# Kernel tuning notes

Hardware: AMD Instinct MI355X
Metric: run time of the kernel (lower is better)

Reference implementation:

```python
import jax, jax.numpy as jnp
import numpy as np

N_NODES = 100000
N_EDGES = 1600000
NUM_GRAPHS = 128


def _gcn_layer(x, W, b, senders, receivers, n_node):
    # Linear transform first (cheaper: feature dim small)
    x = x @ W + b  # [N, out]
    ones = jnp.ones(senders.shape[0], dtype=x.dtype)
    deg_s = jax.ops.segment_sum(ones, senders, n_node)     # out-degree
    deg_r = jax.ops.segment_sum(ones, receivers, n_node)   # in-degree
    # symmetric normalization: D^-1/2 A D^-1/2
    x = x * jax.lax.rsqrt(jnp.maximum(deg_s, 1.0))[:, None]
    x = jax.ops.segment_sum(x[senders], receivers, n_node)  # gather-scatter aggregation
    x = x * jax.lax.rsqrt(jnp.maximum(deg_r, 1.0))[:, None]
    return x


def setup_inputs() -> dict:
    key = jax.random.key(0)
    ks = jax.random.split(key, 10)
    x = jax.random.normal(ks[0], (N_NODES, 9), dtype=jnp.float32)
    senders = jax.random.randint(ks[1], (N_EDGES,), 0, N_NODES)
    receivers = jax.random.randint(ks[2], (N_EDGES,), 0, N_NODES)
    batch = jnp.sort(jax.random.randint(ks[3], (N_NODES,), 0, NUM_GRAPHS))
    # learned params (Dense: W [in,out], b [out]) with LeCun-normal-ish scale
    def dense(k, din, dout):
        return jax.random.normal(k, (din, dout), dtype=jnp.float32) / np.sqrt(din)
    W1 = dense(ks[4], 9, 64)
    b1 = jnp.zeros((64,), jnp.float32)
    W2 = dense(ks[5], 64, 128)
    b2 = jnp.zeros((128,), jnp.float32)
    W3 = dense(ks[6], 128, 2)
    b3 = jnp.zeros((2,), jnp.float32)
    return {"x": x, "senders": senders, "receivers": receivers, "batch": batch,
            "num_graphs": NUM_GRAPHS, "W1": W1, "b1": b1, "W2": W2, "b2": b2,
            "W3": W3, "b3": b3}


def reference(x, senders, receivers, batch, num_graphs, W1, b1, W2, b2, W3, b3):
    n_node = x.shape[0]
    x = jax.nn.relu(_gcn_layer(x, W1, b1, senders, receivers, n_node))
    x = jax.nn.relu(_gcn_layer(x, W2, b2, senders, receivers, n_node))
    x = _gcn_layer(x, W3, b3, senders, receivers, n_node)
    # graph-level pooling
    return jax.ops.segment_sum(x, batch, num_graphs)
```

## Files before the change

### kernel.cpp

```cpp
#include <hip/hip_runtime.h>
#include <hip/hip_bf16.h>
#include <cstddef>

#define NBMAX 512
#define BCAP 5120
#define BKCHUNK 3200

typedef unsigned short bf16t;
typedef __attribute__((ext_vector_type(8))) short short8;
typedef __attribute__((ext_vector_type(4))) float f32x4;

static __device__ __forceinline__ float2 up2(unsigned u) {
    return make_float2(__uint_as_float(u << 16), __uint_as_float(u & 0xffff0000u));
}
static __device__ __forceinline__ bf16t f2bf(float f) {
    unsigned u = __float_as_uint(f);
    u += 0x7fffu + ((u >> 16) & 1u);
    return (bf16t)(u >> 16);
}
static __device__ __forceinline__ unsigned pk2(float a, float b) {
    return (unsigned)f2bf(a) | ((unsigned)f2bf(b) << 16);
}

__global__ void k_bucket(const int* __restrict__ S, const int* __restrict__ R,
                         unsigned* __restrict__ bufR, unsigned char* __restrict__ bufS,
                         int* __restrict__ gCntR, int* __restrict__ gCntS,
                         const float* __restrict__ W2, bf16t* __restrict__ W2f,
                         int nE, int nB) {
    __shared__ int histR[NBMAX], lstR[NBMAX], baseR[NBMAX];
    __shared__ int histS[NBMAX], lstS[NBMAX], baseS[NBMAX];
    __shared__ int sm[256];
    __shared__ unsigned sortedR[BKCHUNK];
    __shared__ unsigned short bOfR[BKCHUNK];
    __shared__ unsigned char sortedS[BKCHUNK];
    __shared__ unsigned short bOfS[BKCHUNK];
    int t = threadIdx.x;
    int nSort = gridDim.x - 4;
    if (blockIdx.x >= nSort) {
        int tt = (blockIdx.x - nSort) * blockDim.x + t;
        if (tt < 1024) {
            int nt = tt >> 7, kh = (tt >> 6) & 1, lane = tt & 63;
            int n = nt * 16 + (lane & 15);
            int k0 = kh * 32 + (lane >> 4) * 8;
            uint4 p;
            p.x = pk2(W2[(k0 + 0) * 128 + n], W2[(k0 + 1) * 128 + n]);
            p.y = pk2(W2[(k0 + 2) * 128 + n], W2[(k0 + 3) * 128 + n]);
            p.z = pk2(W2[(k0 + 4) * 128 + n], W2[(k0 + 5) * 128 + n]);
            p.w = pk2(W2[(k0 + 6) * 128 + n], W2[(k0 + 7) * 128 + n]);
            ((uint4*)W2f)[tt] = p;
        }
        return;
    }
    for (int i = t; i < NBMAX; i += 256) { histR[i] = 0; histS[i] = 0; }
    __syncthreads();
    int chunk = (nE + nSort - 1) / nSort;
    int e0 = blockIdx.x * chunk;
    int e1 = min(e0 + chunk, nE);
    for (int e = e0 + t; e < e1; e += 256) {
        atomicAdd(&histR[R[e] >> 8], 1);
        atomicAdd(&histS[S[e] >> 8], 1);
    }
    __syncthreads();
    {
        int c0 = histR[2 * t], c1 = histR[2 * t + 1];
        int ps = c0 + c1;
        sm[t] = ps;
        __syncthreads();
        for (int off = 1; off < 256; off <<= 1) {
            int y = (t >= off) ? sm[t - off] : 0;
            __syncthreads();
            sm[t] += y;
            __syncthreads();
        }
        int ex = sm[t] - ps;
        lstR[2 * t] = ex;
        lstR[2 * t + 1] = ex + c0;
    }
    __syncthreads();
    {
        int c0 = histS[2 * t], c1 = histS[2 * t + 1];
        int ps = c0 + c1;
        sm[t] = ps;
        __syncthreads();
        for (int off = 1; off < 256; off <<= 1) {
            int y = (t >= off) ? sm[t - off] : 0;
            __syncthreads();
            sm[t] += y;
            __syncthreads();
        }
        int ex = sm[t] - ps;
        lstS[2 * t] = ex;
        lstS[2 * t + 1] = ex + c0;
    }
    __syncthreads();
    for (int i = t; i < nB; i += 256) {
        int cR = histR[i];
        baseR[i] = cR ? atomicAdd(&gCntR[i], cR) : 0;
        int cS = histS[i];
        baseS[i] = cS ? atomicAdd(&gCntS[i], cS) : 0;
    }
    for (int i = t; i < NBMAX; i += 256) { histR[i] = 0; histS[i] = 0; }
    __syncthreads();
    for (int e = e0 + t; e < e1; e += 256) {
        int r = R[e], s = S[e];
        int br = r >> 8;
        int p = lstR[br] + atomicAdd(&histR[br], 1);
        sortedR[p] = ((unsigned)(r & 255) << 24) | (unsigned)s;
        bOfR[p] = (unsigned short)br;
        int bs = s >> 8;
        int p2 = lstS[bs] + atomicAdd(&histS[bs], 1);
        sortedS[p2] = (unsigned char)(s & 255);
        bOfS[p2] = (unsigned short)bs;
    }
    __syncthreads();
    int cnt = e1 - e0;
    for (int i = t; i < cnt; i += 256) {
        int b = bOfR[i];
        int slot = baseR[b] + (i - lstR[b]);
        if (slot < BCAP) bufR[(size_t)b * BCAP + slot] = sortedR[i];
        int b2 = bOfS[i];
        int slot2 = baseS[b2] + (i - lstS[b2]);
        if (slot2 < BCAP) bufS[(size_t)b2 * BCAP + slot2] = sortedS[i];
    }
}

__global__ void k_pass2(const unsigned* __restrict__ bufR, const unsigned char* __restrict__ bufS,
                        const int* __restrict__ gCntR, const int* __restrict__ gCntS,
                        const float* __restrict__ x,
                        int* __restrict__ csr, int* __restrict__ cur, int* __restrict__ degR,
                        float* __restrict__ inv_r, float* __restrict__ inv_s,
                        bf16t* __restrict__ xs, int* __restrict__ perm, int nN, int nB) {
    __shared__ int hist[256], incl[256], curs[256], histS[256];
    __shared__ int sm[256];
    __shared__ int gex[NBMAX];
    int t = threadIdx.x;
    int b = blockIdx.x;
    {
        int c0 = (2 * t < nB) ? gCntR[2 * t] : 0;
        int c1 = (2 * t + 1 < nB) ? gCntR[2 * t + 1] : 0;
        int ps = c0 + c1;
        sm[t] = ps;
        __syncthreads();
        for (int off = 1; off < 256; off <<= 1) {
            int y = (t >= off) ? sm[t - off] : 0;
            __syncthreads();
            sm[t] += y;
            __syncthreads();
        }
        int ex = sm[t] - ps;
        gex[2 * t] = ex;
        gex[2 * t + 1] = ex + c0;
    }
    hist[t] = 0; curs[t] = 0; histS[t] = 0;
    __syncthreads();
    int gb = gex[b];
    int cnt = gCntR[b];
    const unsigned* buf = bufR + (size_t)b * BCAP;
    for (int i = t; i < cnt; i += 256) atomicAdd(&hist[buf[i] >> 24], 1);
    __syncthreads();
    int v = hist[t];
    sm[t] = v;
    __syncthreads();
    for (int off = 1; off < 256; off <<= 1) {
        int y = (t >= off) ? sm[t - off] : 0;
        __syncthreads();
        sm[t] += y;
        __syncthreads();
    }
    incl[t] = sm[t];
    __syncthreads();
    int n0 = b << 8;
    int n = n0 + t;
    if (n < nN) {
        degR[n] = v;
        cur[n] = gb + incl[t];
        inv_r[n] = rsqrtf(fmaxf((float)v, 1.f));
    }
    for (int i = t; i < cnt; i += 256) {
        unsigned p = buf[i];
        int rl = p >> 24;
        int s = p & 0xFFFFFF;
        int pos = gb + (incl[rl] - hist[rl]) + atomicAdd(&curs[rl], 1);
        csr[pos] = s;
    }
    int cntS = gCntS[b];
    const unsigned char* bufs = bufS + (size_t)b * BCAP;
    for (int i = t; i < cntS; i += 256) atomicAdd(&histS[bufs[i]], 1);
    __syncthreads();
    if (n < nN) {
        float is = rsqrtf(fmaxf((float)histS[t], 1.f));
        inv_s[n] = is;
        float w[9];
#pragma unroll
        for (int k = 0; k < 9; k++) w[k] = x[(size_t)n * 9 + k] * is;
        uint4 pa, pb;
        pa.x = pk2(w[0], w[1]); pa.y = pk2(w[2], w[3]);
        pa.z = pk2(w[4], w[5]); pa.w = pk2(w[6], w[7]);
        pb.x = pk2(w[8], is);   pb.y = 0; pb.z = 0; pb.w = 0;
        uint4* o = (uint4*)(xs + (size_t)n * 16);
        o[0] = pa;
        o[1] = pb;
    }
    __syncthreads();
    hist[t] = 0;
    curs[t] = 0;
    __syncthreads();
    int nInB = min(nN - n0, 256);
    int dv = 0;
    if (t < nInB) {
        dv = min(v, 255);
        atomicAdd(&hist[dv], 1);
    }
    __syncthreads();
    int hv = hist[t];
    sm[t] = hv;
    __syncthreads();
    for (int off = 1; off < 256; off <<= 1) {
        int y = (t >= off) ? sm[t - off] : 0;
        __syncthreads();
        sm[t] += y;
        __syncthreads();
    }
    if (t < nInB) {
        int pos = (sm[dv] - hist[dv]) + atomicAdd(&curs[dv], 1);
        perm[n0 + pos] = n;
    }
}

__global__ void k_h1f(const unsigned* __restrict__ xs32, const float* __restrict__ W1,
                      const float* __restrict__ b1,
                      const int* __restrict__ csr, const int* __restrict__ cur,
                      const int* __restrict__ degR, const float* __restrict__ inv_r,
                      const float* __restrict__ inv_s, const int* __restrict__ perm,
                      bf16t* __restrict__ h1s, float* __restrict__ warr, int nN) {
    __shared__ float Wl[9 * 64];
    __shared__ float bl[64];
    for (int i = threadIdx.x; i < 9 * 64; i += blockDim.x) Wl[i] = W1[i];
    if (threadIdx.x < 64) bl[threadIdx.x] = b1[threadIdx.x];
    __syncthreads();
    int lane = threadIdx.x & 63;
    int wave = threadIdx.x >> 6;
    int j = blockIdx.x * 16 + wave * 4 + (lane >> 4);
    int jc = min(j, nN - 1);
    int nc = perm[jc];
    int ql = lane & 15;
    int g = ql >> 1;
    int f2 = ql & 1;
    int deg = degR[nc];
    int st = cur[nc] - deg;
    float a0 = 0.f, a1 = 0.f, a2 = 0.f, a3 = 0.f;
    float a4 = 0.f, a5 = 0.f, a6 = 0.f, a7 = 0.f;
    int i = 0;
    for (; i + 16 <= deg; i += 16) {
        int ea = csr[st + i + g];
        int eb = csr[st + i + 8 + g];
        uint4 ua = *(const uint4*)(xs32 + (size_t)ea * 8 + f2 * 4);
        uint4 ub = *(const uint4*)(xs32 + (size_t)eb * 8 + f2 * 4);
        float2 p;
        p = up2(ua.x); a0 += p.x; a1 += p.y;
        p = up2(ua.y); a2 += p.x; a3 += p.y;
        p = up2(ua.z); a4 += p.x; a5 += p.y;
        p = up2(ua.w); a6 += p.x; a7 += p.y;
        p = up2(ub.x); a0 += p.x; a1 += p.y;
        p = up2(ub.y); a2 += p.x; a3 += p.y;
        p = up2(ub.z); a4 += p.x; a5 += p.y;
        p = up2(ub.w); a6 += p.x; a7 += p.y;
    }
    if (i + 8 <= deg) {
        int ea = csr[st + i + g];
        uint4 ua = *(const uint4*)(xs32 + (size_t)ea * 8 + f2 * 4);
        float2 p;
        p = up2(ua.x); a0 += p.x; a1 += p.y;
        p = up2(ua.y); a2 += p.x; a3 += p.y;
        p = up2(ua.z); a4 += p.x; a5 += p.y;
        p = up2(ua.w); a6 += p.x; a7 += p.y;
        i += 8;
    }
    if (g < deg - i) {
        int ea = csr[st + i + g];
        uint4 ua = *(const uint4*)(xs32 + (size_t)ea * 8 + f2 * 4);
        float2 p;
        p = up2(ua.x); a0 += p.x; a1 += p.y;
        p = up2(ua.y); a2 += p.x; a3 += p.y;
        p = up2(ua.z); a4 += p.x; a5 += p.y;
        p = up2(ua.w); a6 += p.x; a7 += p.y;
    }
    a0 += __shfl_xor(a0, 2); a1 += __shfl_xor(a1, 2); a2 += __shfl_xor(a2, 2); a3 += __shfl_xor(a3, 2);
    a4 += __shfl_xor(a4, 2); a5 += __shfl_xor(a5, 2); a6 += __shfl_xor(a6, 2); a7 += __shfl_xor(a7, 2);
    a0 += __shfl_xor(a0, 4); a1 += __shfl_xor(a1, 4); a2 += __shfl_xor(a2, 4); a3 += __shfl_xor(a3, 4);
    a4 += __shfl_xor(a4, 4); a5 += __shfl_xor(a5, 4); a6 += __shfl_xor(a6, 4); a7 += __shfl_xor(a7, 4);
    a0 += __shfl_xor(a0, 8); a1 += __shfl_xor(a1, 8); a2 += __shfl_xor(a2, 8); a3 += __shfl_xor(a3, 8);
    a4 += __shfl_xor(a4, 8); a5 += __shfl_xor(a5, 8); a6 += __shfl_xor(a6, 8); a7 += __shfl_xor(a7, 8);
    int base = lane & 48;
    float xv[9];
    xv[0] = __shfl(a0, base); xv[1] = __shfl(a1, base);
    xv[2] = __shfl(a2, base); xv[3] = __shfl(a3, base);
    xv[4] = __shfl(a4, base); xv[5] = __shfl(a5, base);
    xv[6] = __shfl(a6, base); xv[7] = __shfl(a7, base);
    xv[8] = __shfl(a0, base + 1);
    float w = __shfl(a1, base + 1);
    float ir = inv_r[nc];
    float is = inv_s[nc];
    int c0 = ql * 4;
    float acc[4];
#pragma unroll
    for (int jj = 0; jj < 4; jj++) acc[jj] = w * bl[c0 + jj];
#pragma unroll
    for (int k = 0; k < 9; k++) {
        float4 wv = *(const float4*)(Wl + k * 64 + c0);
        acc[0] += xv[k] * wv.x;
        acc[1] += xv[k] * wv.y;
        acc[2] += xv[k] * wv.z;
        acc[3] += xv[k] * wv.w;
    }
    if (j < nN) {
        float v0 = fmaxf(acc[0] * ir, 0.f) * is;
        float v1 = fmaxf(acc[1] * ir, 0.f) * is;
        float v2 = fmaxf(acc[2] * ir, 0.f) * is;
        float v3 = fmaxf(acc[3] * ir, 0.f) * is;
        uint2 pv;
        pv.x = pk2(v0, v1);
        pv.y = pk2(v2, v3);
        *(uint2*)(h1s + (size_t)nc * 64 + c0) = pv;
        if (ql == 0) warr[nc] = w;
    }
}

__global__ void __launch_bounds__(128, 8)
k_l2f(const unsigned* __restrict__ h32, const bf16t* __restrict__ W2f,
      const float* __restrict__ b2, const float* __restrict__ W3,
      const float* __restrict__ inv_r, const float* __restrict__ inv_s,
      const float* __restrict__ warr,
      const int* __restrict__ csr, const int* __restrict__ cur,
      const int* __restrict__ degR, const int* __restrict__ perm,
      float* __restrict__ t, float* __restrict__ dout, int outSize, int nN) {
    __shared__ float b2l[128];
    __shared__ float W3l[256];
    __shared__ unsigned zl[16 * 36];
    for (int i = threadIdx.x; i < 128; i += blockDim.x) b2l[i] = b2[i];
    for (int i = threadIdx.x; i < 256; i += blockDim.x) W3l[i] = W3[i];
    if (blockIdx.x == 0)
        for (int i = threadIdx.x; i < outSize; i += blockDim.x) dout[i] = 0.f;
    int lane = threadIdx.x & 63;
    int wave = threadIdx.x >> 6;
    int g3 = lane >> 3;
    int sub = lane & 7;
    int n0b = blockIdx.x * 16;
    {
        int roff = wave * 8 + g3;
        int jc = min(n0b + roff, nN - 1);
        int nc = perm[jc];
        int deg = degR[nc];
        int st = cur[nc] - deg;
        float a0 = 0.f, a1 = 0.f, a2 = 0.f, a3 = 0.f;
        float a4 = 0.f, a5 = 0.f, a6 = 0.f, a7 = 0.f;
        int i = 0;
        for (; i + 4 <= deg; i += 4) {
            int e0 = csr[st + i + 0];
            int e1 = csr[st + i + 1];
            int e2 = csr[st + i + 2];
            int e3 = csr[st + i + 3];
            uint4 u0 = *(const uint4*)(h32 + (size_t)e0 * 32 + sub * 4);
            uint4 u1 = *(const uint4*)(h32 + (size_t)e1 * 32 + sub * 4);
            uint4 u2 = *(const uint4*)(h32 + (size_t)e2 * 32 + sub * 4);
            uint4 u3 = *(const uint4*)(h32 + (size_t)e3 * 32 + sub * 4);
            float2 p;
            p = up2(u0.x); a0 += p.x; a1 += p.y;
            p = up2(u0.y); a2 += p.x; a3 += p.y;
            p = up2(u0.z); a4 += p.x; a5 += p.y;
            p = up2(u0.w); a6 += p.x; a7 += p.y;
            p = up2(u1.x); a0 += p.x; a1 += p.y;
            p = up2(u1.y); a2 += p.x; a3 += p.y;
            p = up2(u1.z); a4 += p.x; a5 += p.y;
            p = up2(u1.w); a6 += p.x; a7 += p.y;
            p = up2(u2.x); a0 += p.x; a1 += p.y;
            p = up2(u2.y); a2 += p.x; a3 += p.y;
            p = up2(u2.z); a4 += p.x; a5 += p.y;
            p = up2(u2.w); a6 += p.x; a7 += p.y;
            p = up2(u3.x); a0 += p.x; a1 += p.y;
            p = up2(u3.y); a2 += p.x; a3 += p.y;
            p = up2(u3.z); a4 += p.x; a5 += p.y;
            p = up2(u3.w); a6 += p.x; a7 += p.y;
        }
        for (; i < deg; i++) {
            int e0 = csr[st + i];
            uint4 u0 = *(const uint4*)(h32 + (size_t)e0 * 32 + sub * 4);
            float2 p;
            p = up2(u0.x); a0 += p.x; a1 += p.y;
            p = up2(u0.y); a2 += p.x; a3 += p.y;
            p = up2(u0.z); a4 += p.x; a5 += p.y;
            p = up2(u0.w); a6 += p.x; a7 += p.y;
        }
        uint4 pv;
        pv.x = pk2(a0, a1);
        pv.y = pk2(a2, a3);
        pv.z = pk2(a4, a5);
        pv.w = pk2(a6, a7);
        *(uint4*)(zl + roff * 36 + sub * 4) = pv;
    }
    __syncthreads();
    int m = lane & 15;
    int q = lane >> 4;
    short8 afr0 = *(const short8*)(zl + m * 36 + q * 4);
    short8 afr1 = *(const short8*)(zl + m * 36 + 16 + q * 4);
    float w4[4], ir4[4], is4[4];
    int nr4[4];
#pragma unroll
    for (int reg = 0; reg < 4; reg++) {
        int jr = min(n0b + q * 4 + reg, nN - 1);
        int nr = perm[jr];
        nr4[reg] = nr;
        w4[reg] = warr[nr];
        ir4[reg] = inv_r[nr];
        is4[reg] = inv_s[nr];
    }
    float p0[4] = {0.f, 0.f, 0.f, 0.f}, p1[4] = {0.f, 0.f, 0.f, 0.f};
#pragma unroll
    for (int nt = 0; nt < 8; nt++) {
        short8 b0 = *(const short8*)(W2f + ((size_t)(nt * 2 + 0) * 64 + lane) * 8);
        short8 b1 = *(const short8*)(W2f + ((size_t)(nt * 2 + 1) * 64 + lane) * 8);
        f32x4 acc = {0.f, 0.f, 0.f, 0.f};
        acc = __builtin_amdgcn_mfma_f32_16x16x32_bf16(afr0, b0, acc, 0, 0, 0);
        acc = __builtin_amdgcn_mfma_f32_16x16x32_bf16(afr1, b1, acc, 0, 0, 0);
        int col = nt * 16 + m;
        float bc = b2l[col];
        float w30 = W3l[col * 2 + 0];
        float w31 = W3l[col * 2 + 1];
#pragma unroll
        for (int reg = 0; reg < 4; reg++) {
            float h = fmaxf((acc[reg] + w4[reg] * bc) * ir4[reg], 0.f) * is4[reg];
            p0[reg] += h * w30;
            p1[reg] += h * w31;
        }
    }
#pragma unroll
    for (int mask = 1; mask < 16; mask <<= 1) {
#pragma unroll
        for (int reg = 0; reg < 4; reg++) {
            p0[reg] += __shfl_xor(p0[reg], mask);
            p1[reg] += __shfl_xor(p1[reg], mask);
        }
    }
    if (wave == 0 && m == 0) {
#pragma unroll
        for (int reg = 0; reg < 4; reg++) {
            int jr = n0b + q * 4 + reg;
            if (jr < nN) *(float2*)(t + (size_t)nr4[reg] * 2) = make_float2(p0[reg], p1[reg]);
        }
    }
}

__global__ void k_poolg(const float* __restrict__ t, const float* __restrict__ inv_r,
                        const float* __restrict__ warr, const float* __restrict__ b3,
                        const int* __restrict__ csr, const int* __restrict__ cur,
                        const int* __restrict__ degR, const int* __restrict__ batch,
                        const int* __restrict__ perm,
                        float* out, int nN, int outSize) {
    __shared__ float sm[256];
    for (int i = threadIdx.x; i < 256; i += blockDim.x) sm[i] = 0.f;
    __syncthreads();
    int tid = blockIdx.x * blockDim.x + threadIdx.x;
    int j = tid >> 3;
    int sub = tid & 7;
    if (j < nN) {
        int n = perm[j];
        int deg = degR[n];
        int st = cur[n] - deg;
        float a0 = 0.f, a1 = 0.f, c0 = 0.f, c1 = 0.f;
        int i = sub;
        for (; i + 8 < deg; i += 16) {
            int sa = csr[st + i], sb = csr[st + i + 8];
            float2 va = ((const float2*)t)[sa];
            float2 vb = ((const float2*)t)[sb];
            a0 += va.x; a1 += va.y;
            c0 += vb.x; c1 += vb.y;
        }
        for (; i < deg; i += 8) {
            float2 va = ((const float2*)t)[csr[st + i]];
            a0 += va.x; a1 += va.y;
        }
        float p0 = a0 + c0;
        float p1 = a1 + c1;
        p0 += __shfl_xor(p0, 1); p1 += __shfl_xor(p1, 1);
        p0 += __shfl_xor(p0, 2); p1 += __shfl_xor(p1, 2);
        p0 += __shfl_xor(p0, 4); p1 += __shfl_xor(p1, 4);
        if (sub == 0) {
            float ir = inv_r[n];
            float wb = warr[n] * ir;
            int g = batch[n];
            atomicAdd(&sm[2 * g + 0], p0 * ir + wb * b3[0]);
            atomicAdd(&sm[2 * g + 1], p1 * ir + wb * b3[1]);
        }
    }
    __syncthreads();
    for (int i = threadIdx.x; i < outSize; i += blockDim.x) {
        float v = sm[i];
        if (v != 0.f) atomicAdd(&out[i], v);
    }
}

extern "C" void kernel_launch(void* const* d_in, const int* in_sizes, int n_in,
                              void* d_out, int out_size, void* d_ws, size_t ws_size,
                              hipStream_t stream) {
    const float* x     = (const float*)d_in[0];
    const int*   S     = (const int*)d_in[1];
    const int*   R     = (const int*)d_in[2];
    const int*   batch = (const int*)d_in[3];
    const float* W1 = (const float*)d_in[5];
    const float* b1 = (const float*)d_in[6];
    const float* W2 = (const float*)d_in[7];
    const float* b2 = (const float*)d_in[8];
    const float* W3 = (const float*)d_in[9];
    const float* b3 = (const float*)d_in[10];

    int nN = in_sizes[0] / 9;
    int nE = in_sizes[1];
    int nB = (nN + 255) / 256;

    char* ws = (char*)d_ws;
    int*   cur   = (int*)ws;
    int*   degR  = cur + nN;
    float* inv_s = (float*)(degR + nN);
    float* inv_r = inv_s + nN;
    float* warr  = inv_r + nN;
    int*   perm  = (int*)(warr + nN);
    int*   gCntR = perm + nN;
    int*   gCntS = gCntR + NBMAX;
    int*   csr   = gCntS + NBMAX;
    bf16t* xs    = (bf16t*)(csr + nE);
    bf16t* W2f   = xs + (size_t)nN * 16;
    char*  regA  = (char*)(W2f + 8192);
    unsigned*      bufR = (unsigned*)regA;
    unsigned char* bufS = (unsigned char*)(bufR + (size_t)NBMAX * BCAP);
    bf16t* h1s = (bf16t*)regA;
    float* t   = (float*)(regA + (size_t)NBMAX * BCAP * 5);

    const int B = 256;

    hipMemsetAsync(gCntR, 0, 2 * NBMAX * 4, stream);
    k_bucket<<<516, B, 0, stream>>>(S, R, bufR, bufS, gCntR, gCntS, W2, W2f, nE, nB);
    k_pass2<<<nB, B, 0, stream>>>(bufR, bufS, gCntR, gCntS, x, csr, cur, degR,
                                  inv_r, inv_s, xs, perm, nN, nB);

    k_h1f<<<(nN + 15) / 16, B, 0, stream>>>((const unsigned*)xs, W1, b1, csr, cur, degR,
                                            inv_r, inv_s, perm, h1s, warr, nN);

    k_l2f<<<(nN + 15) / 16, 128, 0, stream>>>((const unsigned*)h1s, W2f, b2, W3,
                                              inv_r, inv_s, warr, csr, cur, degR, perm,
                                              t, (float*)d_out, out_size, nN);

    k_poolg<<<(nN * 8 + B - 1) / B, B, 0, stream>>>(t, inv_r, warr, b3, csr, cur, degR, batch,
                                                    perm, (float*)d_out, nN, out_size);
}
```

Before: 229.0 us.

## Count out-degree with global atomics and drop degree-sorted node permutation

Sender out-degrees are now counted with global atomicAdd into a zeroed per-node array, instead of going through a second bucket sort with shared-memory histograms and a per-bucket byte buffer. The per-bucket permutation that sorted nodes by in-degree is also removed, so the aggregation kernels process nodes in natural order. This cuts shared-memory work, scans and global buffer traffic in the preprocessing kernels. The cost is 1.6M scattered global atomics and less even wave workloads in the gather kernels, since neighbouring nodes no longer have similar degrees.

```diff
diff --git a/kernel.cpp b/kernel.cpp
--- a/kernel.cpp
+++ b/kernel.cpp
@@ -23,17 +23,14 @@
 }
 
 __global__ void k_bucket(const int* __restrict__ S, const int* __restrict__ R,
-                         unsigned* __restrict__ bufR, unsigned char* __restrict__ bufS,
-                         int* __restrict__ gCntR, int* __restrict__ gCntS,
+                         unsigned* __restrict__ bufR, int* __restrict__ degS,
+                         int* __restrict__ gCntR,
                          const float* __restrict__ W2, bf16t* __restrict__ W2f,
                          int nE, int nB) {
     __shared__ int histR[NBMAX], lstR[NBMAX], baseR[NBMAX];
-    __shared__ int histS[NBMAX], lstS[NBMAX], baseS[NBMAX];
     __shared__ int sm[256];
     __shared__ unsigned sortedR[BKCHUNK];
     __shared__ unsigned short bOfR[BKCHUNK];
-    __shared__ unsigned char sortedS[BKCHUNK];
-    __shared__ unsigned short bOfS[BKCHUNK];
     int t = threadIdx.x;
     int nSort = gridDim.x - 4;
     if (blockIdx.x >= nSort) {
@@ -51,14 +48,14 @@
         }
         return;
     }
-    for (int i = t; i < NBMAX; i += 256) { histR[i] = 0; histS[i] = 0; }
+    for (int i = t; i < NBMAX; i += 256) histR[i] = 0;
     __syncthreads();
     int chunk = (nE + nSort - 1) / nSort;
     int e0 = blockIdx.x * chunk;
     int e1 = min(e0 + chunk, nE);
     for (int e = e0 + t; e < e1; e += 256) {
         atomicAdd(&histR[R[e] >> 8], 1);
-        atomicAdd(&histS[S[e] >> 8], 1);
+        atomicAdd(&degS[S[e]], 1);
     }
     __syncthreads();
     {
@@ -77,29 +74,11 @@
         lstR[2 * t + 1] = ex + c0;
     }
     __syncthreads();
-    {
-        int c0 = histS[2 * t], c1 = histS[2 * t + 1];
-        int ps = c0 + c1;
-        sm[t] = ps;
-        __syncthreads();
-        for (int off = 1; off < 256; off <<= 1) {
-            int y = (t >= off) ? sm[t - off] : 0;
-            __syncthreads();
-            sm[t] += y;
-            __syncthreads();
-        }
-        int ex = sm[t] - ps;
-        lstS[2 * t] = ex;
-        lstS[2 * t + 1] = ex + c0;
-    }
-    __syncthreads();
     for (int i = t; i < nB; i += 256) {
         int cR = histR[i];
         baseR[i] = cR ? atomicAdd(&gCntR[i], cR) : 0;
-        int cS = histS[i];
-        baseS[i] = cS ? atomicAdd(&gCntS[i], cS) : 0;
-    }
-    for (int i = t; i < NBMAX; i += 256) { histR[i] = 0; histS[i] = 0; }
+    }
+    for (int i = t; i < NBMAX; i += 256) histR[i] = 0;
     __syncthreads();
     for (int e = e0 + t; e < e1; e += 256) {
         int r = R[e], s = S[e];
@@ -107,10 +86,6 @@
         int p = lstR[br] + atomicAdd(&histR[br], 1);
         sortedR[p] = ((unsigned)(r & 255) << 24) | (unsigned)s;
         bOfR[p] = (unsigned short)br;
-        int bs = s >> 8;
-        int p2 = lstS[bs] + atomicAdd(&histS[bs], 1);
-        sortedS[p2] = (unsigned char)(s & 255);
-        bOfS[p2] = (unsigned short)bs;
     }
     __syncthreads();
     int cnt = e1 - e0;
@@ -118,19 +93,15 @@
         int b = bOfR[i];
         int slot = baseR[b] + (i - lstR[b]);
         if (slot < BCAP) bufR[(size_t)b * BCAP + slot] = sortedR[i];
-        int b2 = bOfS[i];
-        int slot2 = baseS[b2] + (i - lstS[b2]);
-        if (slot2 < BCAP) bufS[(size_t)b2 * BCAP + slot2] = sortedS[i];
-    }
-}
-
-__global__ void k_pass2(const unsigned* __restrict__ bufR, const unsigned char* __restrict__ bufS,
-                        const int* __restrict__ gCntR, const int* __restrict__ gCntS,
-                        const float* __restrict__ x,
+    }
+}
+
+__global__ void k_pass2(const unsigned* __restrict__ bufR, const int* __restrict__ gCntR,
+                        const int* __restrict__ degS, const float* __restrict__ x,
                         int* __restrict__ csr, int* __restrict__ cur, int* __restrict__ degR,
                         float* __restrict__ inv_r, float* __restrict__ inv_s,
-                        bf16t* __restrict__ xs, int* __restrict__ perm, int nN, int nB) {
-    __shared__ int hist[256], incl[256], curs[256], histS[256];
+                        bf16t* __restrict__ xs, int nN, int nB) {
+    __shared__ int hist[256], incl[256], curs[256];
     __shared__ int sm[256];
     __shared__ int gex[NBMAX];
     int t = threadIdx.x;
@@ -151,7 +122,7 @@
         gex[2 * t] = ex;
         gex[2 * t + 1] = ex + c0;
     }
-    hist[t] = 0; curs[t] = 0; histS[t] = 0;
+    hist[t] = 0; curs[t] = 0;
     __syncthreads();
     int gb = gex[b];
     int cnt = gCntR[b];
@@ -183,12 +154,8 @@
         int pos = gb + (incl[rl] - hist[rl]) + atomicAdd(&curs[rl], 1);
         csr[pos] = s;
     }
-    int cntS = gCntS[b];
-    const unsigned char* bufs = bufS + (size_t)b * BCAP;
-    for (int i = t; i < cntS; i += 256) atomicAdd(&histS[bufs[i]], 1);
-    __syncthreads();
     if (n < nN) {
-        float is = rsqrtf(fmaxf((float)histS[t], 1.f));
+        float is = rsqrtf(fmaxf((float)degS[n], 1.f));
         inv_s[n] = is;
         float w[9];
 #pragma unroll
@@ -201,37 +168,13 @@
         o[0] = pa;
         o[1] = pb;
     }
-    __syncthreads();
-    hist[t] = 0;
-    curs[t] = 0;
-    __syncthreads();
-    int nInB = min(nN - n0, 256);
-    int dv = 0;
-    if (t < nInB) {
-        dv = min(v, 255);
-        atomicAdd(&hist[dv], 1);
-    }
-    __syncthreads();
-    int hv = hist[t];
-    sm[t] = hv;
-    __syncthreads();
-    for (int off = 1; off < 256; off <<= 1) {
-        int y = (t >= off) ? sm[t - off] : 0;
-        __syncthreads();
-        sm[t] += y;
-        __syncthreads();
-    }
-    if (t < nInB) {
-        int pos = (sm[dv] - hist[dv]) + atomicAdd(&curs[dv], 1);
-        perm[n0 + pos] = n;
-    }
 }
 
 __global__ void k_h1f(const unsigned* __restrict__ xs32, const float* __restrict__ W1,
                       const float* __restrict__ b1,
                       const int* __restrict__ csr, const int* __restrict__ cur,
                       const int* __restrict__ degR, const float* __restrict__ inv_r,
-                      const float* __restrict__ inv_s, const int* __restrict__ perm,
+                      const float* __restrict__ inv_s,
                       bf16t* __restrict__ h1s, float* __restrict__ warr, int nN) {
     __shared__ float Wl[9 * 64];
     __shared__ float bl[64];
@@ -240,9 +183,8 @@
     __syncthreads();
     int lane = threadIdx.x & 63;
     int wave = threadIdx.x >> 6;
-    int j = blockIdx.x * 16 + wave * 4 + (lane >> 4);
-    int jc = min(j, nN - 1);
-    int nc = perm[jc];
+    int n = blockIdx.x * 16 + wave * 4 + (lane >> 4);
+    int nc = min(n, nN - 1);
     int ql = lane & 15;
     int g = ql >> 1;
     int f2 = ql & 1;
@@ -313,7 +255,7 @@
         acc[2] += xv[k] * wv.z;
         acc[3] += xv[k] * wv.w;
     }
-    if (j < nN) {
+    if (n < nN) {
         float v0 = fmaxf(acc[0] * ir, 0.f) * is;
         float v1 = fmaxf(acc[1] * ir, 0.f) * is;
         float v2 = fmaxf(acc[2] * ir, 0.f) * is;
@@ -321,8 +263,8 @@
         uint2 pv;
         pv.x = pk2(v0, v1);
         pv.y = pk2(v2, v3);
-        *(uint2*)(h1s + (size_t)nc * 64 + c0) = pv;
-        if (ql == 0) warr[nc] = w;
+        *(uint2*)(h1s + (size_t)n * 64 + c0) = pv;
+        if (ql == 0) warr[n] = w;
     }
 }
 
@@ -332,7 +274,7 @@
       const float* __restrict__ inv_r, const float* __restrict__ inv_s,
       const float* __restrict__ warr,
       const int* __restrict__ csr, const int* __restrict__ cur,
-      const int* __restrict__ degR, const int* __restrict__ perm,
+      const int* __restrict__ degR,
       float* __restrict__ t, float* __restrict__ dout, int outSize, int nN) {
     __shared__ float b2l[128];
     __shared__ float W3l[256];
@@ -348,8 +290,7 @@
     int n0b = blockIdx.x * 16;
     {
         int roff = wave * 8 + g3;
-        int jc = min(n0b + roff, nN - 1);
-        int nc = perm[jc];
+        int nc = min(n0b + roff, nN - 1);
         int deg = degR[nc];
         int st = cur[nc] - deg;
         float a0 = 0.f, a1 = 0.f, a2 = 0.f, a3 = 0.f;
@@ -404,12 +345,9 @@
     short8 afr0 = *(const short8*)(zl + m * 36 + q * 4);
     short8 afr1 = *(const short8*)(zl + m * 36 + 16 + q * 4);
     float w4[4], ir4[4], is4[4];
-    int nr4[4];
 #pragma unroll
     for (int reg = 0; reg < 4; reg++) {
-        int jr = min(n0b + q * 4 + reg, nN - 1);
-        int nr = perm[jr];
-        nr4[reg] = nr;
+        int nr = min(n0b + q * 4 + reg, nN - 1);
         w4[reg] = warr[nr];
         ir4[reg] = inv_r[nr];
         is4[reg] = inv_s[nr];
@@ -444,8 +382,8 @@
     if (wave == 0 && m == 0) {
 #pragma unroll
         for (int reg = 0; reg < 4; reg++) {
-            int jr = n0b + q * 4 + reg;
-            if (jr < nN) *(float2*)(t + (size_t)nr4[reg] * 2) = make_float2(p0[reg], p1[reg]);
+            int nr = n0b + q * 4 + reg;
+            if (nr < nN) *(float2*)(t + (size_t)nr * 2) = make_float2(p0[reg], p1[reg]);
         }
     }
 }
@@ -454,16 +392,14 @@
                         const float* __restrict__ warr, const float* __restrict__ b3,
                         const int* __restrict__ csr, const int* __restrict__ cur,
                         const int* __restrict__ degR, const int* __restrict__ batch,
-                        const int* __restrict__ perm,
                         float* out, int nN, int outSize) {
     __shared__ float sm[256];
     for (int i = threadIdx.x; i < 256; i += blockDim.x) sm[i] = 0.f;
     __syncthreads();
     int tid = blockIdx.x * blockDim.x + threadIdx.x;
-    int j = tid >> 3;
+    int n = tid >> 3;
     int sub = tid & 7;
-    if (j < nN) {
-        int n = perm[j];
+    if (n < nN) {
         int deg = degR[n];
         int st = cur[n] - deg;
         float a0 = 0.f, a1 = 0.f, c0 = 0.f, c1 = 0.f;
@@ -523,32 +459,30 @@
     float* inv_s = (float*)(degR + nN);
     float* inv_r = inv_s + nN;
     float* warr  = inv_r + nN;
-    int*   perm  = (int*)(warr + nN);
-    int*   gCntR = perm + nN;
-    int*   gCntS = gCntR + NBMAX;
-    int*   csr   = gCntS + NBMAX;
+    int*   degS  = (int*)(warr + nN);
+    int*   gCntR = degS + nN;
+    int*   csr   = gCntR + NBMAX;
     bf16t* xs    = (bf16t*)(csr + nE);
     bf16t* W2f   = xs + (size_t)nN * 16;
     char*  regA  = (char*)(W2f + 8192);
-    unsigned*      bufR = (unsigned*)regA;
-    unsigned char* bufS = (unsigned char*)(bufR + (size_t)NBMAX * BCAP);
+    unsigned* bufR = (unsigned*)regA;
     bf16t* h1s = (bf16t*)regA;
     float* t   = (float*)(regA + (size_t)NBMAX * BCAP * 5);
 
     const int B = 256;
 
-    hipMemsetAsync(gCntR, 0, 2 * NBMAX * 4, stream);
-    k_bucket<<<516, B, 0, stream>>>(S, R, bufR, bufS, gCntR, gCntS, W2, W2f, nE, nB);
-    k_pass2<<<nB, B, 0, stream>>>(bufR, bufS, gCntR, gCntS, x, csr, cur, degR,
-                                  inv_r, inv_s, xs, perm, nN, nB);
+    hipMemsetAsync(degS, 0, (size_t)(nN + NBMAX) * 4, stream);
+    k_bucket<<<516, B, 0, stream>>>(S, R, bufR, degS, gCntR, W2, W2f, nE, nB);
+    k_pass2<<<nB, B, 0, stream>>>(bufR, gCntR, degS, x, csr, cur, degR,
+                                  inv_r, inv_s, xs, nN, nB);
 
     k_h1f<<<(nN + 15) / 16, B, 0, stream>>>((const unsigned*)xs, W1, b1, csr, cur, degR,
-                                            inv_r, inv_s, perm, h1s, warr, nN);
+                                            inv_r, inv_s, h1s, warr, nN);
 
     k_l2f<<<(nN + 15) / 16, 128, 0, stream>>>((const unsigned*)h1s, W2f, b2, W3,
-                                              inv_r, inv_s, warr, csr, cur, degR, perm,
+                                              inv_r, inv_s, warr, csr, cur, degR,
                                               t, (float*)d_out, out_size, nN);
 
     k_poolg<<<(nN * 8 + B - 1) / B, B, 0, stream>>>(t, inv_r, warr, b3, csr, cur, degR, batch,
-                                                    perm, (float*)d_out, nN, out_size);
-}
+                                                    (float*)d_out, nN, out_size);
+}
```

Measured after the change: 255.7 us. +11.7%, slower.
